# Optimization experiments

Measured on AMD Instinct MI355X. Metric: run time of the kernel, lower is better.

Reference implementation:

```python
import jax, jax.numpy as jnp
import numpy as np

B, C, I, E = 2048, 256, 9, 10


def _contraction(U_list, W_list, x, y):
    """Recursive symmetric contraction for one output irrep.
    U_list/W_list ordered [U1, U2, U3] (correlation 1..3).
    x: [b, c, i], y: [b, e]. Returns flattened [b, c * m].
    """
    U3, W3 = U_list[-1], W_list[-1]
    # main: '...ik,ekc,bci,be->bc...'
    out = jnp.einsum('...ik,ekc,bci,be->bc...', U3, W3, x, y)
    for corr in range(len(U_list) - 2, -1, -1):
        U, W = U_list[corr], W_list[corr]
        # weighting: '...k,ekc,be->bc...'
        c_tensor = jnp.einsum('...k,ekc,be->bc...', U, W, y) + out
        # contract: 'bc...i,bci->bc...'
        out = jnp.einsum('bc...i,bci->bc...', c_tensor, x)
    return out.reshape(out.shape[0], -1)


def setup_inputs() -> dict:
    key = jax.random.key(0)
    ks = jax.random.split(key, 14)
    inp = {
        'x': jax.random.normal(ks[0], (B, C, I), jnp.float32),
        'y': jax.random.uniform(ks[1], (B, E), jnp.float32),
        'U1_s': jax.random.normal(ks[2], (I, 1), jnp.float32),
        'U2_s': jax.random.normal(ks[3], (I, I, 3), jnp.float32),
        'U3_s': jax.random.normal(ks[4], (I, I, I, 23), jnp.float32),
        'U1_v': jax.random.normal(ks[5], (3, I, 1), jnp.float32),
        'U2_v': jax.random.normal(ks[6], (3, I, I, 4), jnp.float32),
        'U3_v': jax.random.normal(ks[7], (3, I, I, I, 30), jnp.float32),
        'W1_s': jax.random.normal(ks[8], (E, 1, C), jnp.float32),
        'W2_s': jax.random.normal(ks[9], (E, 3, C), jnp.float32) / 3.0,
        'W3_s': jax.random.normal(ks[10], (E, 23, C), jnp.float32) / 23.0,
        'W1_v': jax.random.normal(ks[11], (E, 1, C), jnp.float32),
        'W2_v': jax.random.normal(ks[12], (E, 4, C), jnp.float32) / 4.0,
        'W3_v': jax.random.normal(ks[13], (E, 30, C), jnp.float32) / 30.0,
    }
    return inp


def reference(x, y, U1_s, U2_s, U3_s, U1_v, U2_v, U3_v,
              W1_s, W2_s, W3_s, W1_v, W2_v, W3_v):
    out_s = _contraction([U1_s, U2_s, U3_s], [W1_s, W2_s, W3_s], x, y)  # [b, c]
    out_v = _contraction([U1_v, U2_v, U3_v], [W1_v, W2_v, W3_v], x, y)  # [b, c*3]
    return jnp.concatenate([out_s, out_v], axis=-1)  # [b, 4c]
```

## Files before the change

### kernel.cpp

```cpp
#include <hip/hip_runtime.h>
#include <hip/hip_bf16.h>


#define NB 2048
#define NC 256
#define NI 9
#define NE 10

#define N_TRI 165
#define N_PAIR 45
#define BT 8

#define T3N (N_TRI * NE * NC)
#define T2N (N_PAIR * NE * NC)
#define T1N (NI * NE * NC)

__global__ __launch_bounds__(256) void sc_prep(
    const float* __restrict__ U1_s, const float* __restrict__ U2_s,
    const float* __restrict__ U3_s, const float* __restrict__ U1_v,
    const float* __restrict__ U2_v, const float* __restrict__ U3_v,
    const float* __restrict__ W1_s, const float* __restrict__ W2_s,
    const float* __restrict__ W3_s, const float* __restrict__ W1_v,
    const float* __restrict__ W2_v, const float* __restrict__ W3_v,
    float* __restrict__ ws)
{
    const int m = blockIdx.x;
    const int e = blockIdx.y;
    const int tid = threadIdx.x;
    float4* __restrict__ T3 = (float4*)ws;
    float4* __restrict__ T2 = T3 + T3N;
    float4* __restrict__ T1 = T2 + T2N;

    __shared__ float sym[128];

    if (m < N_TRI) {
        if (tid < 113) {
            int ii = 0, jj = 0, kk = 0, cnt = 0;
            for (int i = 0; i < NI; i++)
                for (int j = i; j < NI; j++)
                    for (int k = j; k < NI; k++) {
                        if (cnt == m) { ii = i; jj = j; kk = k; }
                        cnt++;
                    }
            int P[6][3]; int np;
            if (ii == jj && jj == kk) {
                np = 1;
                P[0][0] = ii; P[0][1] = ii; P[0][2] = ii;
            } else if (ii == jj) {
                np = 3;
                P[0][0] = ii; P[0][1] = ii; P[0][2] = kk;
                P[1][0] = ii; P[1][1] = kk; P[1][2] = ii;
                P[2][0] = kk; P[2][1] = ii; P[2][2] = ii;
            } else if (jj == kk) {
                np = 3;
                P[0][0] = ii; P[0][1] = jj; P[0][2] = jj;
                P[1][0] = jj; P[1][1] = ii; P[1][2] = jj;
                P[2][0] = jj; P[2][1] = jj; P[2][2] = ii;
            } else {
                np = 6;
                P[0][0] = ii; P[0][1] = jj; P[0][2] = kk;
                P[1][0] = ii; P[1][1] = kk; P[1][2] = jj;
                P[2][0] = jj; P[2][1] = ii; P[2][2] = kk;
                P[3][0] = jj; P[3][1] = kk; P[3][2] = ii;
                P[4][0] = kk; P[4][1] = ii; P[4][2] = jj;
                P[5][0] = kk; P[5][1] = jj; P[5][2] = ii;
            }
            float s = 0.f;
            if (tid < 23) {
                for (int p = 0; p < np; p++)
                    s += U3_s[((P[p][0] * NI + P[p][1]) * NI + P[p][2]) * 23 + tid];
            } else {
                int a = (tid - 23) / 30, t = (tid - 23) % 30;
                for (int p = 0; p < np; p++)
                    s += U3_v[(((a * NI + P[p][0]) * NI + P[p][1]) * NI + P[p][2]) * 30 + t];
            }
            sym[tid] = s;
        }
        __syncthreads();
        const int c = tid;
        float s = 0.f, v0 = 0.f, v1 = 0.f, v2 = 0.f;
        #pragma unroll
        for (int t = 0; t < 23; t++)
            s = fmaf(sym[t], W3_s[(e * 23 + t) * NC + c], s);
        #pragma unroll
        for (int t = 0; t < 30; t++) {
            float wv = W3_v[(e * 30 + t) * NC + c];
            v0 = fmaf(sym[23 + t], wv, v0);
            v1 = fmaf(sym[53 + t], wv, v1);
            v2 = fmaf(sym[83 + t], wv, v2);
        }
        T3[(m * NE + e) * NC + c] = make_float4(s, v0, v1, v2);
    } else if (m < N_TRI + N_PAIR) {
        const int mm = m - N_TRI;
        if (tid < 15) {
            int ii = 0, jj = 0, cnt = 0;
            for (int i = 0; i < NI; i++)
                for (int j = i; j < NI; j++) {
                    if (cnt == mm) { ii = i; jj = j; }
                    cnt++;
                }
            float s;
            if (tid < 3) {
                s = U2_s[(ii * NI + jj) * 3 + tid];
                if (ii != jj) s += U2_s[(jj * NI + ii) * 3 + tid];
            } else {
                int a = (tid - 3) / 4, t = (tid - 3) % 4;
                s = U2_v[((a * NI + ii) * NI + jj) * 4 + t];
                if (ii != jj) s += U2_v[((a * NI + jj) * NI + ii) * 4 + t];
            }
            sym[tid] = s;
        }
        __syncthreads();
        const int c = tid;
        float s = 0.f, v0 = 0.f, v1 = 0.f, v2 = 0.f;
        #pragma unroll
        for (int t = 0; t < 3; t++)
            s = fmaf(sym[t], W2_s[(e * 3 + t) * NC + c], s);
        #pragma unroll
        for (int t = 0; t < 4; t++) {
            float wv = W2_v[(e * 4 + t) * NC + c];
            v0 = fmaf(sym[3 + t],  wv, v0);
            v1 = fmaf(sym[7 + t],  wv, v1);
            v2 = fmaf(sym[11 + t], wv, v2);
        }
        T2[(mm * NE + e) * NC + c] = make_float4(s, v0, v1, v2);
    } else {
        const int i = m - N_TRI - N_PAIR;
        const int c = tid;
        float w1s = W1_s[e * NC + c], w1v = W1_v[e * NC + c];
        T1[(i * NE + e) * NC + c] = make_float4(
            U1_s[i] * w1s,
            U1_v[0 * NI + i] * w1v,
            U1_v[1 * NI + i] * w1v,
            U1_v[2 * NI + i] * w1v);
    }
}

#define ROW_TB(BUF, PHI_EXPR)                                     \
    {                                                             \
        _Pragma("unroll")                                         \
        for (int n = 0; n < BT; n++) {                            \
            const float phi = (PHI_EXPR);                         \
            float t0 = 0.f, t1 = 0.f, t2 = 0.f, t3 = 0.f;         \
            _Pragma("unroll")                                     \
            for (int e = 0; e < NE; e++) {                        \
                const float we = w[e][n];                         \
                t0 = fmaf(we, BUF[e].x, t0);                      \
                t1 = fmaf(we, BUF[e].y, t1);                      \
                t2 = fmaf(we, BUF[e].z, t2);                      \
                t3 = fmaf(we, BUF[e].w, t3);                      \
            }                                                     \
            acc[n][0] = fmaf(phi, t0, acc[n][0]);                 \
            acc[n][1] = fmaf(phi, t1, acc[n][1]);                 \
            acc[n][2] = fmaf(phi, t2, acc[n][2]);                 \
            acc[n][3] = fmaf(phi, t3, acc[n][3]);                 \
        }                                                         \
    }

template <int M0, int M1, int I0, int J0, int K0>
__device__ __forceinline__ void do_triples(
    const float4* __restrict__ T3, int c, const float* __restrict__ xb,
    const float (&w)[NE][BT], float (&acc)[BT][4])
{
    int i = I0, j = J0, k = K0;
    float pij[BT];
    #pragma unroll
    for (int n = 0; n < BT; n++)
        pij[n] = xb[(i * BT + n) * 64] * xb[(j * BT + n) * 64];
    for (int m = M0; ; ) {
        float4 buf[NE];
        #pragma unroll
        for (int e = 0; e < NE; e++) buf[e] = T3[(m * NE + e) * NC + c];
        ROW_TB(buf, pij[n] * xb[(k * BT + n) * 64])
        if (++m == M1) break;
        k++;
        if (k == NI) {
            j++;
            if (j == NI) { i++; j = i; }
            k = j;
            #pragma unroll
            for (int n = 0; n < BT; n++)
                pij[n] = xb[(i * BT + n) * 64] * xb[(j * BT + n) * 64];
        }
    }
}

__global__ __launch_bounds__(256) void sc_main(
    const float* __restrict__ x, const float* __restrict__ y,
    const float* __restrict__ ws, float* __restrict__ out)
{
    const int tid = threadIdx.x;
    const int tx  = tid & 63;
    const int wv  = __builtin_amdgcn_readfirstlane(tid >> 6);
    const int bid = blockIdx.x;
    const int xcd    = bid & 7;
    const int c_tile = xcd >> 1;
    const int b_tile = ((bid >> 3) << 1) | (xcd & 1);
    const int c0 = c_tile << 6;
    const int c  = c0 + tx;
    const int b0 = b_tile << 3;

    __shared__ float xs[NI][BT][64];
    __shared__ float red[BT][4][64];

    #pragma unroll
    for (int p = 0; p < 2; p++) {
        const int pair = tid + p * 256;
        const int n = pair >> 6, cc = pair & 63;
        const float* xp = x + ((size_t)(b0 + n) * NC + c0 + cc) * NI;
        #pragma unroll
        for (int i = 0; i < NI; i++) xs[i][n][cc] = xp[i];
    }
    __syncthreads();
    const float* xb = &xs[0][0][tx];

    float w[NE][BT];
    #pragma unroll
    for (int n = 0; n < BT; n++)
        #pragma unroll
        for (int e = 0; e < NE; e++) w[e][n] = y[(b0 + n) * NE + e];

    float acc[BT][4];
    #pragma unroll
    for (int n = 0; n < BT; n++)
        #pragma unroll
        for (int h = 0; h < 4; h++) acc[n][h] = 0.f;

    const float4* __restrict__ T3 = (const float4*)ws;
    const float4* __restrict__ T2 = T3 + T3N;
    const float4* __restrict__ T1 = T2 + T2N;

    if (wv == 0) {
        do_triples<0, 55, 0, 0, 0>(T3, c, xb, w, acc);
    } else if (wv == 1) {
        do_triples<55, 110, 1, 2, 4>(T3, c, xb, w, acc);
    } else if (wv == 2) {
        do_triples<110, N_TRI, 3, 3, 4>(T3, c, xb, w, acc);
    } else {
        {
            int i = 0, j = 0;
            float pi[BT];
            #pragma unroll
            for (int n = 0; n < BT; n++) pi[n] = xb[n * 64];
            for (int m = 0; ; ) {
                float4 buf[NE];
                #pragma unroll
                for (int e = 0; e < NE; e++) buf[e] = T2[(m * NE + e) * NC + c];
                ROW_TB(buf, pi[n] * xb[(j * BT + n) * 64])
                if (++m == N_PAIR) break;
                j++;
                if (j == NI) {
                    i++; j = i;
                    #pragma unroll
                    for (int n = 0; n < BT; n++)
                        pi[n] = xb[(i * BT + n) * 64];
                }
            }
        }
        for (int i = 0; i < NI; i++) {
            float4 buf[NE];
            #pragma unroll
            for (int e = 0; e < NE; e++) buf[e] = T1[(i * NE + e) * NC + c];
            ROW_TB(buf, xb[(i * BT + n) * 64])
        }
    }

    if (wv == 0) {
        #pragma unroll
        for (int n = 0; n < BT; n++)
            #pragma unroll
            for (int h = 0; h < 4; h++) red[n][h][tx] = acc[n][h];
    }
    __syncthreads();
    if (wv == 1) {
        #pragma unroll
        for (int n = 0; n < BT; n++)
            #pragma unroll
            for (int h = 0; h < 4; h++) acc[n][h] += red[n][h][tx];
    }
    __syncthreads();
    if (wv == 1) {
        #pragma unroll
        for (int n = 0; n < BT; n++)
            #pragma unroll
            for (int h = 0; h < 4; h++) red[n][h][tx] = acc[n][h];
    }
    __syncthreads();
    if (wv == 2) {
        #pragma unroll
        for (int n = 0; n < BT; n++)
            #pragma unroll
            for (int h = 0; h < 4; h++) acc[n][h] += red[n][h][tx];
    }
    __syncthreads();
    if (wv == 2) {
        #pragma unroll
        for (int n = 0; n < BT; n++)
            #pragma unroll
            for (int h = 0; h < 4; h++) red[n][h][tx] = acc[n][h];
    }
    __syncthreads();
    if (wv == 3) {
        #pragma unroll
        for (int n = 0; n < BT; n++) {
            float* ob = out + (size_t)(b0 + n) * (4 * NC);
            ob[c]              = acc[n][0] + red[n][0][tx];
            ob[NC + 3 * c + 0] = acc[n][1] + red[n][1][tx];
            ob[NC + 3 * c + 1] = acc[n][2] + red[n][2][tx];
            ob[NC + 3 * c + 2] = acc[n][3] + red[n][3][tx];
        }
    }
}

extern "C" void kernel_launch(void* const* d_in, const int* in_sizes, int n_in,
                              void* d_out, int out_size, void* d_ws, size_t ws_size,
                              hipStream_t stream) {
    const float* x    = (const float*)d_in[0];
    const float* y    = (const float*)d_in[1];
    const float* U1_s = (const float*)d_in[2];
    const float* U2_s = (const float*)d_in[3];
    const float* U3_s = (const float*)d_in[4];
    const float* U1_v = (const float*)d_in[5];
    const float* U2_v = (const float*)d_in[6];
    const float* U3_v = (const float*)d_in[7];
    const float* W1_s = (const float*)d_in[8];
    const float* W2_s = (const float*)d_in[9];
    const float* W3_s = (const float*)d_in[10];
    const float* W1_v = (const float*)d_in[11];
    const float* W2_v = (const float*)d_in[12];
    const float* W3_v = (const float*)d_in[13];
    float* out = (float*)d_out;
    float* ws  = (float*)d_ws;

    sc_prep<<<dim3(N_TRI + N_PAIR + NI, NE), 256, 0, stream>>>(
        U1_s, U2_s, U3_s, U1_v, U2_v, U3_v,
        W1_s, W2_s, W3_s, W1_v, W2_v, W3_v, ws);
    sc_main<<<1024, 256, 0, stream>>>(x, y, ws, out);
}
```

Before: 303.2 us.

## Halve batch tile, stream table rows per e, and raise occupancy

Cuts the per-block batch tile from 8 to 4 and doubles the grid. The inner loop now streams one float4 table entry per e and accumulates straight into acc using w*phi, so the 10-entry float4 buffer no longer has to be held in registers. A launch_bounds occupancy hint is added to raise waves per SIMD. The prep kernel also replaces its linear triple/pair index search with closed-form counting. In exchange the T tables are reread twice as often across blocks, and the inner loop does more multiplies per FMA.

```diff
diff --git a/kernel.cpp b/kernel.cpp
--- a/kernel.cpp
+++ b/kernel.cpp
@@ -9,7 +9,7 @@
 
 #define N_TRI 165
 #define N_PAIR 45
-#define BT 8
+#define BT 4
 
 #define T3N (N_TRI * NE * NC)
 #define T2N (N_PAIR * NE * NC)
@@ -35,13 +35,19 @@
 
     if (m < N_TRI) {
         if (tid < 113) {
-            int ii = 0, jj = 0, kk = 0, cnt = 0;
-            for (int i = 0; i < NI; i++)
-                for (int j = i; j < NI; j++)
-                    for (int k = j; k < NI; k++) {
-                        if (cnt == m) { ii = i; jj = j; kk = k; }
-                        cnt++;
-                    }
+            int r = m, ii = 0;
+            for (;;) {
+                const int cnt = (NI - ii) * (NI - ii + 1) / 2;
+                if (r < cnt) break;
+                r -= cnt; ii++;
+            }
+            int jj = ii;
+            for (;;) {
+                const int cnt = NI - jj;
+                if (r < cnt) break;
+                r -= cnt; jj++;
+            }
+            const int kk = jj + r;
             int P[6][3]; int np;
             if (ii == jj && jj == kk) {
                 np = 1;
@@ -93,12 +99,13 @@
     } else if (m < N_TRI + N_PAIR) {
         const int mm = m - N_TRI;
         if (tid < 15) {
-            int ii = 0, jj = 0, cnt = 0;
-            for (int i = 0; i < NI; i++)
-                for (int j = i; j < NI; j++) {
-                    if (cnt == mm) { ii = i; jj = j; }
-                    cnt++;
-                }
+            int r = mm, ii = 0;
+            for (;;) {
+                const int cnt = NI - ii;
+                if (r < cnt) break;
+                r -= cnt; ii++;
+            }
+            const int jj = ii + r;
             float s;
             if (tid < 3) {
                 s = U2_s[(ii * NI + jj) * 3 + tid];
@@ -136,24 +143,24 @@
     }
 }
 
-#define ROW_TB(BUF, PHI_EXPR)                                     \
+__device__ __forceinline__ void tri_advance(int& i, int& j, int& k) {
+    k++;
+    if (k == NI) { j++; if (j == NI) { i++; j = i; } k = j; }
+}
+
+#define ROW_STREAM(TBL, ROWIDX)                                   \
     {                                                             \
         _Pragma("unroll")                                         \
-        for (int n = 0; n < BT; n++) {                            \
-            const float phi = (PHI_EXPR);                         \
-            float t0 = 0.f, t1 = 0.f, t2 = 0.f, t3 = 0.f;         \
+        for (int e = 0; e < NE; e++) {                            \
+            const float4 t = TBL[((ROWIDX) * NE + e) * NC + c];   \
             _Pragma("unroll")                                     \
-            for (int e = 0; e < NE; e++) {                        \
-                const float we = w[e][n];                         \
-                t0 = fmaf(we, BUF[e].x, t0);                      \
-                t1 = fmaf(we, BUF[e].y, t1);                      \
-                t2 = fmaf(we, BUF[e].z, t2);                      \
-                t3 = fmaf(we, BUF[e].w, t3);                      \
+            for (int n = 0; n < BT; n++) {                        \
+                const float p = w[e][n] * phi[n];                 \
+                acc[n][0] = fmaf(p, t.x, acc[n][0]);              \
+                acc[n][1] = fmaf(p, t.y, acc[n][1]);              \
+                acc[n][2] = fmaf(p, t.z, acc[n][2]);              \
+                acc[n][3] = fmaf(p, t.w, acc[n][3]);              \
             }                                                     \
-            acc[n][0] = fmaf(phi, t0, acc[n][0]);                 \
-            acc[n][1] = fmaf(phi, t1, acc[n][1]);                 \
-            acc[n][2] = fmaf(phi, t2, acc[n][2]);                 \
-            acc[n][3] = fmaf(phi, t3, acc[n][3]);                 \
         }                                                         \
     }
 
@@ -163,29 +170,18 @@
     const float (&w)[NE][BT], float (&acc)[BT][4])
 {
     int i = I0, j = J0, k = K0;
-    float pij[BT];
-    #pragma unroll
-    for (int n = 0; n < BT; n++)
-        pij[n] = xb[(i * BT + n) * 64] * xb[(j * BT + n) * 64];
-    for (int m = M0; ; ) {
-        float4 buf[NE];
-        #pragma unroll
-        for (int e = 0; e < NE; e++) buf[e] = T3[(m * NE + e) * NC + c];
-        ROW_TB(buf, pij[n] * xb[(k * BT + n) * 64])
-        if (++m == M1) break;
-        k++;
-        if (k == NI) {
-            j++;
-            if (j == NI) { i++; j = i; }
-            k = j;
-            #pragma unroll
-            for (int n = 0; n < BT; n++)
-                pij[n] = xb[(i * BT + n) * 64] * xb[(j * BT + n) * 64];
-        }
-    }
-}
-
-__global__ __launch_bounds__(256) void sc_main(
+    for (int m = M0; m < M1; m++) {
+        float phi[BT];
+        #pragma unroll
+        for (int n = 0; n < BT; n++)
+            phi[n] = xb[(i * BT + n) * 64] * xb[(j * BT + n) * 64]
+                   * xb[(k * BT + n) * 64];
+        ROW_STREAM(T3, m)
+        tri_advance(i, j, k);
+    }
+}
+
+__global__ __launch_bounds__(256, 8) void sc_main(
     const float* __restrict__ x, const float* __restrict__ y,
     const float* __restrict__ ws, float* __restrict__ out)
 {
@@ -198,15 +194,13 @@
     const int b_tile = ((bid >> 3) << 1) | (xcd & 1);
     const int c0 = c_tile << 6;
     const int c  = c0 + tx;
-    const int b0 = b_tile << 3;
+    const int b0 = b_tile << 2;
 
     __shared__ float xs[NI][BT][64];
     __shared__ float red[BT][4][64];
 
-    #pragma unroll
-    for (int p = 0; p < 2; p++) {
-        const int pair = tid + p * 256;
-        const int n = pair >> 6, cc = pair & 63;
+    {
+        const int n = tid >> 6, cc = tid & 63;
         const float* xp = x + ((size_t)(b0 + n) * NC + c0 + cc) * NI;
         #pragma unroll
         for (int i = 0; i < NI; i++) xs[i][n][cc] = xp[i];
@@ -239,29 +233,21 @@
     } else {
         {
             int i = 0, j = 0;
-            float pi[BT];
-            #pragma unroll
-            for (int n = 0; n < BT; n++) pi[n] = xb[n * 64];
-            for (int m = 0; ; ) {
-                float4 buf[NE];
+            for (int m = 0; m < N_PAIR; m++) {
+                float phi[BT];
                 #pragma unroll
-                for (int e = 0; e < NE; e++) buf[e] = T2[(m * NE + e) * NC + c];
-                ROW_TB(buf, pi[n] * xb[(j * BT + n) * 64])
-                if (++m == N_PAIR) break;
+                for (int n = 0; n < BT; n++)
+                    phi[n] = xb[(i * BT + n) * 64] * xb[(j * BT + n) * 64];
+                ROW_STREAM(T2, m)
                 j++;
-                if (j == NI) {
-                    i++; j = i;
-                    #pragma unroll
-                    for (int n = 0; n < BT; n++)
-                        pi[n] = xb[(i * BT + n) * 64];
-                }
+                if (j == NI) { i++; j = i; }
             }
         }
         for (int i = 0; i < NI; i++) {
-            float4 buf[NE];
-            #pragma unroll
-            for (int e = 0; e < NE; e++) buf[e] = T1[(i * NE + e) * NC + c];
-            ROW_TB(buf, xb[(i * BT + n) * 64])
+            float phi[BT];
+            #pragma unroll
+            for (int n = 0; n < BT; n++) phi[n] = xb[(i * BT + n) * 64];
+            ROW_STREAM(T1, i)
         }
     }
 
@@ -335,5 +321,5 @@
     sc_prep<<<dim3(N_TRI + N_PAIR + NI, NE), 256, 0, stream>>>(
         U1_s, U2_s, U3_s, U1_v, U2_v, U3_v,
         W1_s, W2_s, W3_s, W1_v, W2_v, W3_v, ws);
-    sc_main<<<1024, 256, 0, stream>>>(x, y, ws, out);
-}
+    sc_main<<<2048, 256, 0, stream>>>(x, y, ws, out);
+}
```

New measurement: 308.9 us. Within noise of the previous version (+1.9%).
